# Kernel optimization log

Measured on AMD Instinct MI355X. Metric: run time of the kernel, lower is better.

The kernel has to match this reference:

```python
import jax, jax.numpy as jnp
import numpy as np

B, C, L_IN, O_CH, K, OG, GROUPS = 8, 256, 4096, 256, 3, 4, 1
HID = 64
STRIDE, PAD, DIL = 1, 1, 1
L_OUT = (L_IN + 2 * PAD - DIL * (K - 1) - 1) // STRIDE + 1  # = 4096


def resize_linear(v, l_out):
    """Linear resize along last axis, align_corners=True (matches F.interpolate bilinear on H=1)."""
    l_in = v.shape[-1]
    pos = jnp.arange(l_out, dtype=v.dtype) * ((l_in - 1) / max(l_out - 1, 1))
    i0 = jnp.floor(pos).astype(jnp.int32)
    i1 = jnp.minimum(i0 + 1, l_in - 1)
    w = (pos - i0).astype(v.dtype)
    return v[..., i0] * (1.0 - w) + v[..., i1] * w


def setup_inputs() -> dict:
    key = jax.random.key(0)
    ks = jax.random.split(key, 6)
    x = jax.random.normal(ks[0], (B, C, L_IN), jnp.float32)
    weight = jax.random.normal(ks[1], (O_CH, C // GROUPS, K), jnp.float32) * 0.02
    bias = jax.random.normal(ks[2], (O_CH,), jnp.float32) * 0.01
    # grouped 1x1 convs stored pre-grouped: [groups, out_per_g, in_per_g]
    w1 = jax.random.normal(ks[3], (OG, HID // OG, C // OG), jnp.float32) * 0.05
    b1 = jnp.zeros((HID,), jnp.float32)
    w2 = jax.random.normal(ks[4], (OG, 3 * K, HID // OG), jnp.float32) * 0.1
    b2 = jnp.zeros((OG * 3 * K,), jnp.float32)
    return {"x": x, "weight": weight, "bias": bias, "w1": w1, "b1": b1, "w2": w2, "b2": b2}


def reference(x, weight, bias, w1, b1, w2, b2):
    Bq, Cq, L = x.shape
    # --- offset/modulator head: two grouped 1x1 convs with GELU ---
    xg = x.reshape(Bq, OG, Cq // OG, L)
    h = jnp.einsum('bgcl,goc->bgol', xg, w1).reshape(Bq, HID, L) + b1[None, :, None]
    h = jax.nn.gelu(h, approximate=False)
    hg = h.reshape(Bq, OG, HID // OG, L)
    om = jnp.einsum('bgcl,goc->bgol', hg, w2).reshape(Bq, OG * 3 * K, L) + b2[None, :, None]
    # torch in-place quirk: offset[:, :, 1, :] = 0 zeroes odd channels of om BEFORE modulator softmax
    om = om.at[:, 1:2 * K:2, :].set(0.0)
    offset_x = om[:, 0:2 * K:2, :]                      # [B, K, L] x-offsets
    mod = jax.nn.softmax(om[:, K:, :], axis=1)[:, :K, :]  # softmax over all OG*3K-K chans, use first K
    # --- build per-tap sampling grid (align_corners=True semantics) ---
    off_i = resize_linear(offset_x * (2.0 / L), L_OUT)   # [B, K, L_OUT]
    mod_i = resize_linear(mod, L_OUT)                    # [B, K, L_OUT]
    base = jnp.linspace(-1.0, 1.0, L_OUT, dtype=x.dtype)  # [L_OUT]
    kp = jnp.linspace(-0.5, 0.5, K, dtype=x.dtype)        # [K]
    grid = base[None, None, :] + kp[None, :, None] + off_i  # [B, K, L_OUT]
    pos = (grid + 1.0) * 0.5 * (L - 1)                   # pixel coords
    i0 = jnp.floor(pos).astype(jnp.int32)
    i1 = i0 + 1
    w = pos - i0.astype(x.dtype)                         # [B, K, L_OUT]
    v0 = ((i0 >= 0) & (i0 < L)).astype(x.dtype)
    v1 = ((i1 >= 0) & (i1 < L)).astype(x.dtype)
    i0c = jnp.clip(i0, 0, L - 1)
    i1c = jnp.clip(i1, 0, L - 1)
    gather = jax.vmap(lambda xb, ib: xb[:, ib])          # [C,L],[K,L_OUT] -> [C,K,L_OUT]
    g0 = gather(x, i0c)                                  # [B, C, K, L_OUT]
    g1 = gather(x, i1c)
    sampled = g0 * ((1.0 - w) * v0)[:, None] + g1 * (w * v1)[:, None]  # zeros padding bilinear
    sampled = sampled * mod_i[:, None]                   # modulation
    # --- tap-wise grouped conv accumulate ---
    sg = sampled.reshape(Bq, GROUPS, Cq // GROUPS, K, L_OUT)
    wg = weight.reshape(GROUPS, O_CH // GROUPS, Cq // GROUPS, K)
    out = jnp.einsum('bgckl,gock->bgol', sg, wg).reshape(Bq, O_CH, L_OUT)
    return out + bias[None, :, None]
```

## Files before the change

### kernel.cpp

```cpp
#include <hip/hip_runtime.h>
#include <hip/hip_bf16.h>
#include <math.h>

#define B_    8
#define C_    256
#define L_    4096
#define OCH_  256

typedef __attribute__((ext_vector_type(8)))  short bf16x8;
typedef __attribute__((ext_vector_type(16))) float f32x16;
typedef __attribute__((ext_vector_type(4)))  int   i32x4;

static __device__ __forceinline__ unsigned short bf16_rne(float f) {
    unsigned u = __float_as_uint(f);
    unsigned r = u + 0x7FFFu + ((u >> 16) & 1u);
    return (unsigned short)(r >> 16);
}

static __device__ __forceinline__ void gload_lds16(const void* g, void* l) {
    __builtin_amdgcn_global_load_lds(
        (const __attribute__((address_space(1))) unsigned int*)g,
        (__attribute__((address_space(3))) unsigned int*)l, 16, 0, 0);
}

__global__ __launch_bounds__(512) void k_offsets(
        const float* __restrict__ x,
        const float* __restrict__ w1, const float* __restrict__ b1,
        const float* __restrict__ w2, const float* __restrict__ b2,
        const float* __restrict__ W,  unsigned short* __restrict__ Wb,
        float4* __restrict__ coef) {
    __shared__ float sH[2][4][16][65];
    __shared__ float sOm[64][37];
    int tid  = threadIdx.x;
    int blk  = blockIdx.x;

    if (tid < 384) {
        int i = blk * 384 + tid;
        int k = i % 3;
        int c = (i / 3) & 255;
        int o = i / 768;
        Wb[o * 768 + k * 256 + c] = bf16_rne(W[i]);
    }

    int l    = tid & 63;
    int g    = (tid >> 6) & 3;
    int half = tid >> 8;
    int b    = blk & 7;
    int l0   = (blk >> 3) << 6;
    int lg   = l0 + l;

    const float* xg = x + (size_t)b * C_ * L_ + (size_t)(g * 64 + half * 32) * L_ + lg;

    float h[16];
    #pragma unroll
    for (int o = 0; o < 16; ++o) h[o] = half ? 0.0f : b1[g * 16 + o];
    #pragma unroll 4
    for (int cg = 0; cg < 32; ++cg) {
        float xv = xg[(size_t)cg * L_];
        const float* w1p = w1 + (g * 16) * 64 + half * 32 + cg;
        #pragma unroll
        for (int o = 0; o < 16; ++o) h[o] = fmaf(xv, w1p[o * 64], h[o]);
    }
    #pragma unroll
    for (int o = 0; o < 16; ++o) sH[half][g][o][l] = h[o];
    __syncthreads();

    if (half == 0) {
        float om9[9];
        #pragma unroll
        for (int j = 0; j < 9; ++j) om9[j] = b2[g * 9 + j];
        #pragma unroll
        for (int o = 0; o < 16; ++o) {
            float a  = h[o] + sH[1][g][o][l];
            float hv = 0.5f * a * (1.0f + erff(a * 0.70710678118654752f));
            const float* w2p = w2 + g * 144 + o;
            #pragma unroll
            for (int j = 0; j < 9; ++j) om9[j] = fmaf(hv, w2p[j * 16], om9[j]);
        }
        #pragma unroll
        for (int j = 0; j < 9; ++j) sOm[l][g * 9 + j] = om9[j];
    }
    __syncthreads();
    if (tid >= 64) return;

    float om[36];
    #pragma unroll
    for (int j = 0; j < 36; ++j) om[j] = sOm[tid][j];
    om[1] = 0.0f; om[3] = 0.0f; om[5] = 0.0f;
    float m = om[3];
    #pragma unroll
    for (int j = 4; j < 36; ++j) m = fmaxf(m, om[j]);
    float ssum = 0.0f;
    #pragma unroll
    for (int j = 3; j < 36; ++j) ssum += expf(om[j] - m);
    float inv = 1.0f / ssum;

    int lpos = l0 + tid;
    float base = -1.0f + 2.0f * (float)lpos / (float)(L_ - 1);
    #pragma unroll
    for (int t = 0; t < 3; ++t) {
        float mod  = expf(om[3 + t] - m) * inv;
        float off  = om[2 * t] * (2.0f / (float)L_);
        float grid = base + (-0.5f + 0.5f * (float)t) + off;
        float pp   = (grid + 1.0f) * 0.5f * (float)(L_ - 1);
        float fp   = floorf(pp);
        int i0 = (int)fp, i1 = i0 + 1;
        float w = pp - fp;
        float c0 = (i0 >= 0 && i0 < L_) ? (1.0f - w) * mod : 0.0f;
        float c1 = (i1 >= 0 && i1 < L_) ? w * mod : 0.0f;
        int i0c  = min(max(i0, 0), L_ - 1);
        int i1c  = min(max(i1, 0), L_ - 1);
        int i0f2 = min(max(i0, 0), L_ - 2);
        float d0 = (i0c == i0f2     ? c0 : 0.0f) + (i1c == i0f2     ? c1 : 0.0f);
        float d1 = (i0c == i0f2 + 1 ? c0 : 0.0f) + (i1c == i0f2 + 1 ? c1 : 0.0f);
        coef[((size_t)b * 3 + t) * L_ + lpos] =
            make_float4(d0, d1, __int_as_float(i0f2), 0.0f);
    }
}

__global__ __launch_bounds__(512) void k_sample(
        const float* __restrict__ x, const float4* __restrict__ coef,
        i32x4* __restrict__ Sg) {
    int tid  = threadIdx.x;
    int l    = tid & 127;
    int unit = tid >> 7;
    int bid  = blockIdx.x;
    int b    = bid & 7;
    int r    = bid >> 3;
    int lt   = r & 31;
    int sg   = r >> 5;
    int s    = sg * 4 + unit;
    int tap  = s >> 5;
    int c0   = s * 8 - tap * 256;
    int lgl  = lt * 128 + l;
    const float* xb = x + (size_t)b * C_ * L_;

    float4 cf = coef[((size_t)b * 3 + tap) * L_ + lgl];
    float d0 = cf.x, d1 = cf.y;
    const float* xp = xb + (size_t)c0 * L_ + __float_as_int(cf.z);
    union { unsigned short us[8]; i32x4 v; } pk;
    #pragma unroll
    for (int e = 0; e < 8; ++e) {
        float g0 = xp[0], g1 = xp[1];
        pk.us[e] = bf16_rne(fmaf(g1, d1, g0 * d0));
        xp += L_;
    }
    Sg[((size_t)(b * 32 + lt) * 96 + s) * 128 + l] = pk.v;
}

__global__ __launch_bounds__(512, 4) void k_gemm(
        const unsigned short* __restrict__ Wb,
        const float* __restrict__ bias,
        const i32x4* __restrict__ Sg,
        float* __restrict__ out) {
    __shared__ i32x4 sS[2][8][128];

    const int tid  = threadIdx.x;
    const int lane = tid & 63;
    const int wv   = tid >> 6;
    const int blk  = blockIdx.x;
    const int b    = blk & 7;
    const int lt   = blk >> 3;
    const int l0   = lt * 128;
    const int q    = lane >> 5;
    const int l31  = lane & 31;

    const i32x4* Sblk = Sg + (size_t)(b * 32 + lt) * (96 * 128);
    const unsigned short* WA = Wb + (size_t)(wv * 32 + l31) * 768 + q * 8;

    f32x16 acc0, acc1, acc2, acc3;
    #pragma unroll
    for (int i = 0; i < 16; ++i) { acc0[i] = 0.f; acc1[i] = 0.f; acc2[i] = 0.f; acc3[i] = 0.f; }

    bf16x8 aP0, aP1, aP2, aP3, aQ0, aQ1, aQ2, aQ3;

    aP0 = *(const bf16x8*)(WA);
    aP1 = *(const bf16x8*)(WA + 16);
    aP2 = *(const bf16x8*)(WA + 32);
    aP3 = *(const bf16x8*)(WA + 48);
    gload_lds16(Sblk + tid,       &sS[0][0][0] + tid);
    gload_lds16(Sblk + 512 + tid, &sS[0][0][0] + 512 + tid);

    #pragma unroll
    for (int ch = 0; ch < 12; ++ch) {
        const int buf = ch & 1;

        if (ch < 11) {
            const unsigned short* wn = WA + (ch + 1) * 64;
            aQ0 = *(const bf16x8*)(wn);
            aQ1 = *(const bf16x8*)(wn + 16);
            aQ2 = *(const bf16x8*)(wn + 32);
            aQ3 = *(const bf16x8*)(wn + 48);
        }
        __builtin_amdgcn_sched_barrier(0);

        if (ch < 11) asm volatile("s_waitcnt vmcnt(4)" ::: "memory");
        else         asm volatile("s_waitcnt vmcnt(0)" ::: "memory");
        __builtin_amdgcn_sched_barrier(0);
        __builtin_amdgcn_s_barrier();
        __builtin_amdgcn_sched_barrier(0);

        if (ch < 11) {
            const i32x4* src = Sblk + (ch + 1) * 1024;
            gload_lds16(src + tid,       &sS[buf ^ 1][0][0] + tid);
            gload_lds16(src + 512 + tid, &sS[buf ^ 1][0][0] + 512 + tid);
        }
        __builtin_amdgcn_sched_barrier(0);

        #define KS_STEP(ks, AP) {                                            \
            const i32x4* bp = &sS[buf][(ks) * 2 + q][l31];                   \
            bf16x8 b0 = *(const bf16x8*)(bp);                                \
            bf16x8 b1 = *(const bf16x8*)(bp + 32);                           \
            bf16x8 b2 = *(const bf16x8*)(bp + 64);                           \
            bf16x8 b3 = *(const bf16x8*)(bp + 96);                           \
            __builtin_amdgcn_s_setprio(1);                                   \
            acc0 = __builtin_amdgcn_mfma_f32_32x32x16_bf16(AP, b0, acc0, 0, 0, 0); \
            acc1 = __builtin_amdgcn_mfma_f32_32x32x16_bf16(AP, b1, acc1, 0, 0, 0); \
            acc2 = __builtin_amdgcn_mfma_f32_32x32x16_bf16(AP, b2, acc2, 0, 0, 0); \
            acc3 = __builtin_amdgcn_mfma_f32_32x32x16_bf16(AP, b3, acc3, 0, 0, 0); \
            __builtin_amdgcn_s_setprio(0);                                   \
        }
        KS_STEP(0, aP0)
        KS_STEP(1, aP1)
        KS_STEP(2, aP2)
        KS_STEP(3, aP3)
        #undef KS_STEP

        if (ch < 11) { aP0 = aQ0; aP1 = aQ1; aP2 = aQ2; aP3 = aQ3; }
    }

    #pragma unroll
    for (int reg = 0; reg < 16; ++reg) {
        int rr = (reg & 3) + 8 * (reg >> 2) + 4 * q;
        int o  = wv * 32 + rr;
        float bv = bias[o];
        float* op = out + ((size_t)b * 256 + o) * L_ + l0 + l31;
        op[0]  = acc0[reg] + bv;
        op[32] = acc1[reg] + bv;
        op[64] = acc2[reg] + bv;
        op[96] = acc3[reg] + bv;
    }
}

extern "C" void kernel_launch(void* const* d_in, const int* in_sizes, int n_in,
                              void* d_out, int out_size, void* d_ws, size_t ws_size,
                              hipStream_t stream) {
    const float* x      = (const float*)d_in[0];
    const float* weight = (const float*)d_in[1];
    const float* bias   = (const float*)d_in[2];
    const float* w1     = (const float*)d_in[3];
    const float* b1     = (const float*)d_in[4];
    const float* w2     = (const float*)d_in[5];
    const float* b2     = (const float*)d_in[6];
    float* out = (float*)d_out;

    const size_t COEF_B = (size_t)B_ * 3 * L_ * sizeof(float4);
    const size_t W_B    = (size_t)OCH_ * 768 * 2;
    char* ws = (char*)d_ws;
    float4*         coef = (float4*)ws;
    unsigned short* Wb   = (unsigned short*)(ws + COEF_B);
    i32x4*          Sg   = (i32x4*)(ws + COEF_B + W_B);

    k_offsets<<<B_ * (L_ / 64), 512, 0, stream>>>(x, w1, b1, w2, b2,
                                                  weight, Wb, coef);
    k_sample<<<B_ * 32 * 24, 512, 0, stream>>>(x, coef, Sg);
    k_gemm<<<B_ * (L_ / 128), 512, 0, stream>>>(Wb, bias, Sg, out);
}
```

Before: 76.27 us.

## Fuse bilinear sampling into the MFMA GEMM kernel, dropping the intermediate buffer

```diff
diff --git a/kernel.cpp b/kernel.cpp
--- a/kernel.cpp
+++ b/kernel.cpp
@@ -15,12 +15,6 @@
     unsigned u = __float_as_uint(f);
     unsigned r = u + 0x7FFFu + ((u >> 16) & 1u);
     return (unsigned short)(r >> 16);
-}
-
-static __device__ __forceinline__ void gload_lds16(const void* g, void* l) {
-    __builtin_amdgcn_global_load_lds(
-        (const __attribute__((address_space(1))) unsigned int*)g,
-        (__attribute__((address_space(3))) unsigned int*)l, 16, 0, 0);
 }
 
 __global__ __launch_bounds__(512) void k_offsets(
@@ -118,40 +112,11 @@
     }
 }
 
-__global__ __launch_bounds__(512) void k_sample(
-        const float* __restrict__ x, const float4* __restrict__ coef,
-        i32x4* __restrict__ Sg) {
-    int tid  = threadIdx.x;
-    int l    = tid & 127;
-    int unit = tid >> 7;
-    int bid  = blockIdx.x;
-    int b    = bid & 7;
-    int r    = bid >> 3;
-    int lt   = r & 31;
-    int sg   = r >> 5;
-    int s    = sg * 4 + unit;
-    int tap  = s >> 5;
-    int c0   = s * 8 - tap * 256;
-    int lgl  = lt * 128 + l;
-    const float* xb = x + (size_t)b * C_ * L_;
-
-    float4 cf = coef[((size_t)b * 3 + tap) * L_ + lgl];
-    float d0 = cf.x, d1 = cf.y;
-    const float* xp = xb + (size_t)c0 * L_ + __float_as_int(cf.z);
-    union { unsigned short us[8]; i32x4 v; } pk;
-    #pragma unroll
-    for (int e = 0; e < 8; ++e) {
-        float g0 = xp[0], g1 = xp[1];
-        pk.us[e] = bf16_rne(fmaf(g1, d1, g0 * d0));
-        xp += L_;
-    }
-    Sg[((size_t)(b * 32 + lt) * 96 + s) * 128 + l] = pk.v;
-}
-
-__global__ __launch_bounds__(512, 4) void k_gemm(
+__global__ __launch_bounds__(512, 2) void k_conv(
+        const float* __restrict__ x,
         const unsigned short* __restrict__ Wb,
         const float* __restrict__ bias,
-        const i32x4* __restrict__ Sg,
+        const float4* __restrict__ coef,
         float* __restrict__ out) {
     __shared__ i32x4 sS[2][8][128];
 
@@ -164,8 +129,19 @@
     const int l0   = lt * 128;
     const int q    = lane >> 5;
     const int l31  = lane & 31;
-
-    const i32x4* Sblk = Sg + (size_t)(b * 32 + lt) * (96 * 128);
+    const int ls   = tid & 127;
+    const int su   = tid >> 7;
+
+    const float* xb = x + (size_t)b * (C_ * L_);
+
+    float4 cf0 = coef[((size_t)b * 3 + 0) * L_ + l0 + ls];
+    float4 cf1 = coef[((size_t)b * 3 + 1) * L_ + l0 + ls];
+    float4 cf2 = coef[((size_t)b * 3 + 2) * L_ + l0 + ls];
+    const int   ib0 = __float_as_int(cf0.z), ib1 = __float_as_int(cf1.z), ib2 = __float_as_int(cf2.z);
+    const float d00 = cf0.x, d01 = cf0.y;
+    const float d10 = cf1.x, d11 = cf1.y;
+    const float d20 = cf2.x, d21 = cf2.y;
+
     const unsigned short* WA = Wb + (size_t)(wv * 32 + l31) * 768 + q * 8;
 
     f32x16 acc0, acc1, acc2, acc3;
@@ -173,13 +149,40 @@
     for (int i = 0; i < 16; ++i) { acc0[i] = 0.f; acc1[i] = 0.f; acc2[i] = 0.f; acc3[i] = 0.f; }
 
     bf16x8 aP0, aP1, aP2, aP3, aQ0, aQ1, aQ2, aQ3;
+    float g0a[8], g1a[8], g0b[8], g1b[8];
+    float dA0, dA1, dB0, dB1;
+
+    #define GATHER(CH, SL, G0, G1, D0, D1) {                                  \
+        int s_   = (CH) * 8 + (SL);                                           \
+        int tap_ = s_ >> 5;                                                   \
+        int c0_  = s_ * 8 - tap_ * 256;                                       \
+        int ib_  = tap_ == 2 ? ib2 : tap_ == 1 ? ib1 : ib0;                   \
+        D0 = tap_ == 2 ? d20 : tap_ == 1 ? d10 : d00;                         \
+        D1 = tap_ == 2 ? d21 : tap_ == 1 ? d11 : d01;                         \
+        const float* xp_ = xb + (size_t)c0_ * L_ + ib_;                       \
+        _Pragma("unroll")                                                     \
+        for (int j = 0; j < 8; ++j) {                                         \
+            G0[j] = xp_[(size_t)j * L_];                                      \
+            G1[j] = xp_[(size_t)j * L_ + 1];                                  \
+        }                                                                     \
+    }
+    #define PACK(NBUF, SL, G0, G1, D0, D1) {                                  \
+        union { unsigned short us[8]; i32x4 v; } ph_;                         \
+        _Pragma("unroll")                                                     \
+        for (int e = 0; e < 8; ++e)                                           \
+            ph_.us[e] = bf16_rne(fmaf(G1[e], D1, G0[e] * D0));                \
+        sS[NBUF][SL][ls] = ph_.v;                                             \
+    }
 
     aP0 = *(const bf16x8*)(WA);
     aP1 = *(const bf16x8*)(WA + 16);
     aP2 = *(const bf16x8*)(WA + 32);
     aP3 = *(const bf16x8*)(WA + 48);
-    gload_lds16(Sblk + tid,       &sS[0][0][0] + tid);
-    gload_lds16(Sblk + 512 + tid, &sS[0][0][0] + 512 + tid);
+    GATHER(0, su,     g0a, g1a, dA0, dA1)
+    GATHER(0, su + 4, g0b, g1b, dB0, dB1)
+    PACK(0, su,     g0a, g1a, dA0, dA1)
+    PACK(0, su + 4, g0b, g1b, dB0, dB1)
+    __syncthreads();
 
     #pragma unroll
     for (int ch = 0; ch < 12; ++ch) {
@@ -191,19 +194,8 @@
             aQ1 = *(const bf16x8*)(wn + 16);
             aQ2 = *(const bf16x8*)(wn + 32);
             aQ3 = *(const bf16x8*)(wn + 48);
-        }
-        __builtin_amdgcn_sched_barrier(0);
-
-        if (ch < 11) asm volatile("s_waitcnt vmcnt(4)" ::: "memory");
-        else         asm volatile("s_waitcnt vmcnt(0)" ::: "memory");
-        __builtin_amdgcn_sched_barrier(0);
-        __builtin_amdgcn_s_barrier();
-        __builtin_amdgcn_sched_barrier(0);
-
-        if (ch < 11) {
-            const i32x4* src = Sblk + (ch + 1) * 1024;
-            gload_lds16(src + tid,       &sS[buf ^ 1][0][0] + tid);
-            gload_lds16(src + 512 + tid, &sS[buf ^ 1][0][0] + 512 + tid);
+            GATHER(ch + 1, su,     g0a, g1a, dA0, dA1)
+            GATHER(ch + 1, su + 4, g0b, g1b, dB0, dB1)
         }
         __builtin_amdgcn_sched_barrier(0);
 
@@ -225,9 +217,17 @@
         KS_STEP(2, aP2)
         KS_STEP(3, aP3)
         #undef KS_STEP
-
-        if (ch < 11) { aP0 = aQ0; aP1 = aQ1; aP2 = aQ2; aP3 = aQ3; }
-    }
+        __builtin_amdgcn_sched_barrier(0);
+
+        if (ch < 11) {
+            PACK(buf ^ 1, su,     g0a, g1a, dA0, dA1)
+            PACK(buf ^ 1, su + 4, g0b, g1b, dB0, dB1)
+            aP0 = aQ0; aP1 = aQ1; aP2 = aQ2; aP3 = aQ3;
+        }
+        __syncthreads();
+    }
+    #undef GATHER
+    #undef PACK
 
     #pragma unroll
     for (int reg = 0; reg < 16; ++reg) {
@@ -255,14 +255,11 @@
     float* out = (float*)d_out;
 
     const size_t COEF_B = (size_t)B_ * 3 * L_ * sizeof(float4);
-    const size_t W_B    = (size_t)OCH_ * 768 * 2;
     char* ws = (char*)d_ws;
     float4*         coef = (float4*)ws;
     unsigned short* Wb   = (unsigned short*)(ws + COEF_B);
-    i32x4*          Sg   = (i32x4*)(ws + COEF_B + W_B);
 
     k_offsets<<<B_ * (L_ / 64), 512, 0, stream>>>(x, w1, b1, w2, b2,
                                                   weight, Wb, coef);
-    k_sample<<<B_ * 32 * 24, 512, 0, stream>>>(x, coef, Sg);
-    k_gemm<<<B_ * (L_ / 128), 512, 0, stream>>>(Wb, bias, Sg, out);
-}
+    k_conv<<<B_ * (L_ / 128), 512, 0, stream>>>(x, Wb, bias, coef, out);
+}
```

Result: faster. 68.12 us, median of 2 (-10.7%).
